# Kernel optimization log

Measured on AMD Instinct MI355X. Metric: run time of the kernel, lower is better.

Reference implementation:

```python
import jax, jax.numpy as jnp
import numpy as np

N_NODES = 200000
N_EDGES = 1000000
N_Q = 64
N_REL_ROWS = 401  # 2*n_rel + 1
D = 128
A = 64


def setup_inputs() -> dict:
    key = jax.random.key(0)
    ks = jax.random.split(key, 16)
    s = 0.05  # param scale
    return {
        'hidden': jax.random.normal(ks[0], (N_NODES, D), jnp.float32),
        'q_emb': jax.random.normal(ks[1], (N_Q, D), jnp.float32),
        'rela_embed': jax.random.normal(ks[2], (N_REL_ROWS, D), jnp.float32),
        'Ws_w': jax.random.normal(ks[3], (A, D), jnp.float32) * s,
        'Ws_b': jax.random.normal(ks[4], (A,), jnp.float32) * s,
        'Wr_w': jax.random.normal(ks[5], (A, D), jnp.float32) * s,
        'Wq_w': jax.random.normal(ks[6], (A, D), jnp.float32) * s,
        'Wqr_w': jax.random.normal(ks[7], (A, D), jnp.float32) * s,
        'walpha_w': jax.random.normal(ks[8], (1, A), jnp.float32) * s,
        'walpha_b': jax.random.normal(ks[9], (1,), jnp.float32) * s,
        'Wh_w': jax.random.normal(ks[10], (D, D), jnp.float32) * s,
        'r_idx': jax.random.randint(ks[11], (N_EDGES,), 0, N_Q, jnp.int32),
        'rel': jax.random.randint(ks[12], (N_EDGES,), 0, N_REL_ROWS, jnp.int32),
        'sub': jax.random.randint(ks[13], (N_EDGES,), 0, N_NODES, jnp.int32),
        'obj': jax.random.randint(ks[14], (N_EDGES,), 0, N_NODES, jnp.int32),
    }


def reference(hidden, q_emb, rela_embed, Ws_w, Ws_b, Wr_w, Wq_w, Wqr_w,
              walpha_w, walpha_b, Wh_w, r_idx, rel, sub, obj):
    # Gather per-edge features (memory-bound irregular access)
    hs = hidden[sub]          # [E, D]
    hr = rela_embed[rel]      # [E, D]
    h_qr = q_emb[r_idx]       # [E, D]

    # Fused small attention MLP: sigmoid(w_alpha(relu(Ws hs + Wr hr + Wq hq + Wqr (hr*hq))))
    pre = (jnp.einsum('ed,ad->ea', hs, Ws_w) + Ws_b
           + jnp.einsum('ed,ad->ea', hr, Wr_w)
           + jnp.einsum('ed,ad->ea', h_qr, Wq_w)
           + jnp.einsum('ed,ad->ea', hr * h_qr, Wqr_w))  # [E, A]
    alpha = jax.nn.sigmoid(jnp.einsum('ea,oa->eo', jax.nn.relu(pre), walpha_w) + walpha_b)  # [E, 1]

    # Gated message + scatter-sum aggregation per target node
    message = alpha * (hs * hr)                                   # [E, D]
    message_agg = jax.ops.segment_sum(message, obj, num_segments=N_NODES)  # [N, D]

    hidden_new = jax.nn.relu(jnp.einsum('nd,od->no', message_agg, Wh_w))   # [N, D]
    return hidden_new, alpha
```

## Files before the change

### kernel.cpp

```cpp
#include <hip/hip_runtime.h>
#include <hip/hip_bf16.h>
#include <hip/hip_fp8.h>

#define N_NODES 200000
#define N_EDGES 1000000
#define NQ 64
#define NRELR 401
#define DIM 128
#define AA 64
#define NBK 3125
#define CAP 512

typedef __attribute__((ext_vector_type(8))) short short8_t;
typedef __attribute__((ext_vector_type(4))) float f32x4;

static __device__ inline short f2bs(float f) {
  __hip_bfloat16 h = __float2bfloat16(f);
  return __builtin_bit_cast(short, h);
}
static __device__ inline float bs2f(unsigned short u) {
  unsigned x = ((unsigned)u) << 16;
  return __builtin_bit_cast(float, x);
}
static __device__ inline unsigned pk2(float lo, float hi) {
  unsigned short a = (unsigned short)__builtin_bit_cast(short, __float2bfloat16(lo));
  unsigned short b = (unsigned short)__builtin_bit_cast(short, __float2bfloat16(hi));
  return (unsigned)a | ((unsigned)b << 16);
}
static __device__ inline unsigned char f2e4(float f) {
  __hip_fp8_e4m3 h(f);
  return (unsigned char)h.__x;
}
static __device__ inline float e42f(unsigned char b) {
  __hip_fp8_e4m3 h;
  h.__x = (__hip_fp8_storage_t)b;
  return (float)h;
}
static __device__ inline void atomic_pk_bf16_s(unsigned voff, unsigned val,
                                               const unsigned short* base) {
  asm volatile("global_atomic_pk_add_bf16 %0, %1, %2"
               :: "v"(voff), "v"(val), "s"((unsigned long long)base) : "memory");
}
static __device__ inline short8_t pack8(float4 a, float4 b) {
  short8_t v;
  v[0] = f2bs(a.x); v[1] = f2bs(a.y); v[2] = f2bs(a.z); v[3] = f2bs(a.w);
  v[4] = f2bs(b.x); v[5] = f2bs(b.y); v[6] = f2bs(b.z); v[7] = f2bs(b.w);
  return v;
}

#define CBK 401
#define SBK 512
__global__ __launch_bounds__(256) void prep_kernel(
    const float* __restrict__ hidden, const float* __restrict__ qemb,
    const float* __restrict__ rela, const float* __restrict__ Ws,
    const float* __restrict__ Wsb, const float* __restrict__ Wr,
    const float* __restrict__ Wq, const float* __restrict__ Wqr,
    const int* __restrict__ obj,
    unsigned char* __restrict__ C8, unsigned char* __restrict__ S8,
    unsigned short* __restrict__ relab, short* __restrict__ hidb,
    int* __restrict__ hist2d, int znum) {
  int b = blockIdx.x;
  int t = threadIdx.x;

  if (b < CBK) {
    __shared__ __hip_bfloat16 hqs[64][136];
    __shared__ __hip_bfloat16 vts[128][72];
    __shared__ float hr_f[128];
    __shared__ float trp[4][64];
    __shared__ float tr_s[64];
    int rho = b;

    if (t < 128) {
      float hv = rela[rho * DIM + t];
      hr_f[t] = hv;
      relab[rho * DIM + t] = (unsigned short)f2bs(hv);
    }
    __syncthreads();
    for (int i = t; i < 64 * 128; i += 256) {
      int q = i >> 7, d = i & 127;
      hqs[q][d] = __float2bfloat16(qemb[i]);
      int a = i >> 7;
      vts[d][a] = __float2bfloat16(Wq[i] + hr_f[d] * Wqr[i]);
    }
    {
      int a = t & 63, qt = t >> 6;
      const float* wr = Wr + a * DIM + qt * 32;
      float p = 0.f;
#pragma unroll 8
      for (int i = 0; i < 32; ++i) p += wr[i] * hr_f[qt * 32 + i];
      trp[qt][a] = p;
    }
    __syncthreads();
    if (t < 64)
      tr_s[t] = trp[0][t] + trp[1][t] + trp[2][t] + trp[3][t] + Wsb[t];
    __syncthreads();

    int qg = t >> 4, ag = t & 15;
    int q0 = qg * 4, a0 = ag * 4;
    float acc[4][4];
#pragma unroll
    for (int i = 0; i < 4; ++i)
#pragma unroll
      for (int j = 0; j < 4; ++j) acc[i][j] = 0.f;
    for (int d = 0; d < DIM; ++d) {
      float hv[4], wv[4];
#pragma unroll
      for (int i = 0; i < 4; ++i) hv[i] = __bfloat162float(hqs[q0 + i][d]);
#pragma unroll
      for (int j = 0; j < 4; ++j) wv[j] = __bfloat162float(vts[d][a0 + j]);
#pragma unroll
      for (int i = 0; i < 4; ++i)
#pragma unroll
        for (int j = 0; j < 4; ++j) acc[i][j] += hv[i] * wv[j];
    }
#pragma unroll
    for (int i = 0; i < 4; ++i)
#pragma unroll
      for (int j = 0; j < 4; ++j) {
        int q = q0 + i, a = a0 + j;
        C8[((size_t)rho * 64 + q) * 64 + a] = f2e4(acc[i][j] + tr_s[a]);
      }
  } else if (b < CBK + SBK) {
    int lane = t & 63;
    int lr = lane & 15, lg = lane >> 4;
    int gw = (b - CBK) * 4 + (t >> 6);
    const int NWV = SBK * 4;

    short8_t bf[4][4];
#pragma unroll
    for (int ot = 0; ot < 4; ++ot)
#pragma unroll
      for (int kt = 0; kt < 4; ++kt) {
        const float* wp = Ws + (size_t)(ot * 16 + lr) * DIM + kt * 32 + lg * 8;
        bf[ot][kt] = pack8(*(const float4*)wp, *(const float4*)(wp + 4));
      }

    for (int tt = gw; tt < N_NODES / 16; tt += NWV) {
      const float* ap = hidden + (size_t)tt * 16 * DIM + (size_t)lr * DIM;
      short8_t a[4];
#pragma unroll
      for (int kt = 0; kt < 4; ++kt) {
        const float* p = ap + kt * 32 + lg * 8;
        a[kt] = pack8(*(const float4*)p, *(const float4*)(p + 4));
        *(short8_t*)(hidb + ((size_t)tt * 16 + lr) * DIM + kt * 32 + lg * 8) = a[kt];
      }
      f32x4 acc[4];
#pragma unroll
      for (int ot = 0; ot < 4; ++ot) {
        acc[ot] = (f32x4){0.f, 0.f, 0.f, 0.f};
#pragma unroll
        for (int kt = 0; kt < 4; ++kt)
          acc[ot] = __builtin_amdgcn_mfma_f32_16x16x32_bf16(a[kt], bf[ot][kt], acc[ot], 0, 0, 0);
      }
#pragma unroll
      for (int ot = 0; ot < 4; ++ot)
#pragma unroll
        for (int r = 0; r < 4; ++r)
          S8[((size_t)tt * 16 + lg * 4 + r) * 64 + ot * 16 + lr] = f2e4(acc[ot][r]);
    }
  } else {
    __shared__ int h[NBK];
    int z = b - CBK - SBK;
    for (int i = t; i < NBK; i += 256) h[i] = 0;
    __syncthreads();
    for (int e = z * 256 + t; e < N_EDGES; e += znum * 256)
      atomicAdd(&h[obj[e] >> 6], 1);
    __syncthreads();
    for (int i = t; i < NBK; i += 256)
      hist2d[(size_t)z * NBK + i] = h[i];
  }
}

__global__ __launch_bounds__(256) void offsetsA_kernel(
    const int* __restrict__ hist2d, int* __restrict__ off2d,
    int* __restrict__ totals, int znum) {
  int b0 = blockIdx.x * 256 + threadIdx.x;
  if (b0 >= NBK) return;
  int run = 0;
  for (int z = 0; z < znum; ++z) {
    int v = hist2d[(size_t)z * NBK + b0];
    off2d[(size_t)z * NBK + b0] = run;
    run += v;
  }
  totals[b0] = run;
}

__global__ __launch_bounds__(256) void scan_kernel(
    const int* __restrict__ totals, int* __restrict__ base) {
  __shared__ int part[256];
  int t = threadIdx.x;
  const int PER = (NBK + 255) / 256;
  int lo = t * PER;
  int loc[PER];
  int s = 0;
#pragma unroll
  for (int k = 0; k < PER; ++k) {
    loc[k] = s;
    int idx = lo + k;
    s += (idx < NBK) ? totals[idx] : 0;
  }
  part[t] = s;
  __syncthreads();
  for (int off = 1; off < 256; off <<= 1) {
    int v = (t >= off) ? part[t - off] : 0;
    __syncthreads();
    part[t] += v;
    __syncthreads();
  }
  int pre = (t == 0) ? 0 : part[t - 1];
#pragma unroll
  for (int k = 0; k < PER; ++k) {
    int idx = lo + k;
    if (idx < NBK) base[idx] = pre + loc[k];
  }
  if (t == 255) base[NBK] = part[255];
}

__global__ __launch_bounds__(256) void scatter3_kernel(
    const int* __restrict__ ridx, const int* __restrict__ rel,
    const int* __restrict__ sub, const int* __restrict__ obj,
    const int* __restrict__ base, const int* __restrict__ off2d,
    uint2* __restrict__ recs, int znum) {
  __shared__ int loff[NBK];
  __shared__ int lcur[NBK];
  int t = threadIdx.x, z = blockIdx.x;
  for (int i = t; i < NBK; i += 256) {
    loff[i] = base[i] + off2d[(size_t)z * NBK + i];
    lcur[i] = 0;
  }
  __syncthreads();
  for (int e = z * 256 + t; e < N_EDGES; e += znum * 256) {
    int s = sub[e], r = rel[e], q = ridx[e], o = obj[e];
    int bb = o >> 6;
    int rq = r * 64 + q;
    int p = loff[bb] + atomicAdd(&lcur[bb], 1);
    uint2 rc;
    rc.x = (unsigned)s | ((unsigned)(o & 63) << 18) | ((unsigned)(rq & 0xFF) << 24);
    rc.y = (unsigned)(rq >> 8) | ((unsigned)e << 7);
    recs[p] = rc;
  }
}

__global__ __launch_bounds__(256) void bucket2_kernel(
    const unsigned* __restrict__ hid32, const unsigned* __restrict__ rel32,
    const unsigned char* __restrict__ S8, const unsigned char* __restrict__ C8,
    const float* __restrict__ wal, const float* __restrict__ walb,
    const int* __restrict__ base, const uint2* __restrict__ recs,
    unsigned* __restrict__ agg32, float* __restrict__ alpha_out) {
  __shared__ uint2 lrec[CAP];
  __shared__ unsigned short ord[CAP];
  __shared__ int cnt2[64];
  __shared__ int scn[65];
  __shared__ int curs[64];
  int t = threadIdx.x, b = blockIdx.x;
  int lane = t & 63, w = t >> 6;
  int lo = base[b], hi = base[b + 1];
  int cnt = hi - lo;
  int nbase = b * 64;
  float wa = wal[lane];
  float wb = walb[0];

  if (t < 64) cnt2[t] = 0;
  __syncthreads();

  if (cnt <= CAP) {
    for (int i = t; i < cnt; i += 256) {
      uint2 rc = recs[lo + i];
      lrec[i] = rc;
      atomicAdd(&cnt2[(rc.x >> 18) & 63], 1);
    }
    __syncthreads();
    if (t < 64) scn[t + 1] = cnt2[t];
    if (t == 0) scn[0] = 0;
    __syncthreads();
    for (int off = 1; off < 64; off <<= 1) {
      int v = 0;
      if (t < 64) { v = scn[t + 1]; if (t + 1 > off) v += scn[t + 1 - off]; }
      __syncthreads();
      if (t < 64) scn[t + 1] = v;
      __syncthreads();
    }
    if (t < 64) curs[t] = scn[t];
    __syncthreads();
    for (int i = t; i < cnt; i += 256) {
      int oin = (lrec[i].x >> 18) & 63;
      int p = atomicAdd(&curs[oin], 1);
      ord[p] = (unsigned short)i;
    }
    __syncthreads();

    int n0 = w * 16;
    int s0 = scn[n0], s1 = scn[n0 + 16];
    float m0 = 0.f, m1 = 0.f;
    int curn = -1;
    for (int j = s0; j < s1; j += 4) {
      int nv = s1 - j;
      if (nv > 4) nv = 4;
      int sdx[4], on[4], rq[4], ei[4];
      float y[4], h0[4], h1[4], g0[4], g1[4];
#pragma unroll
      for (int u = 0; u < 4; ++u) {
        int idx = (u < nv) ? (j + u) : j;
        uint2 rc = lrec[ord[idx]];
        unsigned rx = __builtin_amdgcn_readfirstlane(rc.x);
        unsigned ry = __builtin_amdgcn_readfirstlane(rc.y);
        sdx[u] = rx & 0x3FFFF;
        on[u] = (rx >> 18) & 63;
        rq[u] = ((rx >> 24) & 0xFF) | ((ry & 0x7F) << 8);
        ei[u] = ry >> 7;
      }
#pragma unroll
      for (int u = 0; u < 4; ++u) {
        float x = e42f(S8[(size_t)sdx[u] * 64 + lane]) +
                  e42f(C8[(size_t)rq[u] * 64 + lane]);
        y[u] = fmaxf(x, 0.f) * wa;
      }
#pragma unroll
      for (int u = 0; u < 4; ++u) {
        unsigned hp = hid32[(size_t)sdx[u] * 64 + lane];
        unsigned rp = rel32[(size_t)(rq[u] >> 6) * 64 + lane];
        h0[u] = bs2f((unsigned short)(hp & 0xffff));
        h1[u] = bs2f((unsigned short)(hp >> 16));
        g0[u] = bs2f((unsigned short)(rp & 0xffff));
        g1[u] = bs2f((unsigned short)(rp >> 16));
      }
#pragma unroll
      for (int off = 32; off; off >>= 1) {
#pragma unroll
        for (int u = 0; u < 4; ++u) y[u] += __shfl_xor(y[u], off);
      }
#pragma unroll
      for (int u = 0; u < 4; ++u) {
        if (u < nv) {
          float al = 1.f / (1.f + __expf(-(y[u] + wb)));
          if (on[u] != curn) {
            if (curn >= 0)
              agg32[(size_t)(nbase + curn) * 64 + lane] = pk2(m0, m1);
            curn = on[u];
            m0 = 0.f; m1 = 0.f;
          }
          m0 += al * h0[u] * g0[u];
          m1 += al * h1[u] * g1[u];
          if (lane == 0) alpha_out[ei[u]] = al;
        }
      }
    }
    if (curn >= 0)
      agg32[(size_t)(nbase + curn) * 64 + lane] = pk2(m0, m1);
    for (int n = n0; n < n0 + 16; ++n) {
      if (cnt2[n] == 0)
        agg32[(size_t)(nbase + n) * 64 + lane] = 0u;
    }
  } else {
    for (int n = w; n < 64; n += 4)
      agg32[(size_t)(nbase + n) * 64 + lane] = 0u;
    __syncthreads();
    unsigned voff = (unsigned)lane * 4;
    for (int i = lo + w * 4; i < hi; i += 16) {
      int nv = hi - i;
      if (nv > 4) nv = 4;
      for (int u = 0; u < 4; ++u) {
        if (u >= nv) break;
        uint2 rc = recs[i + u];
        unsigned rx = __builtin_amdgcn_readfirstlane(rc.x);
        unsigned ry = __builtin_amdgcn_readfirstlane(rc.y);
        int sdx = rx & 0x3FFFF;
        int on = (rx >> 18) & 63;
        int rq = ((rx >> 24) & 0xFF) | ((ry & 0x7F) << 8);
        int ei = ry >> 7;
        float x = e42f(S8[(size_t)sdx * 64 + lane]) + e42f(C8[(size_t)rq * 64 + lane]);
        float y = fmaxf(x, 0.f) * wa;
        for (int off = 32; off; off >>= 1) y += __shfl_xor(y, off);
        float al = 1.f / (1.f + __expf(-(y + wb)));
        unsigned hp = hid32[(size_t)sdx * 64 + lane];
        unsigned rp = rel32[(size_t)(rq >> 6) * 64 + lane];
        float v0 = al * bs2f((unsigned short)(hp & 0xffff)) * bs2f((unsigned short)(rp & 0xffff));
        float v1 = al * bs2f((unsigned short)(hp >> 16)) * bs2f((unsigned short)(rp >> 16));
        atomic_pk_bf16_s(voff, pk2(v0, v1), (const unsigned short*)(agg32 + (size_t)(nbase + on) * 64));
        if (lane == 0) alpha_out[ei] = al;
      }
    }
  }
}

__global__ __launch_bounds__(256) void out_gemm_bf(
    const float* __restrict__ Wh, const short* __restrict__ aggb,
    float* __restrict__ out) {
  int lane = threadIdx.x & 63;
  int lr = lane & 15, lg = lane >> 4;
  int gw = (blockIdx.x * blockDim.x + threadIdx.x) >> 6;
  int nwv = (gridDim.x * blockDim.x) >> 6;

  short8_t b[8][4];
#pragma unroll
  for (int ot = 0; ot < 8; ++ot)
#pragma unroll
    for (int kt = 0; kt < 4; ++kt) {
      const float* wp = Wh + (size_t)(ot * 16 + lr) * DIM + kt * 32 + lg * 8;
      b[ot][kt] = pack8(*(const float4*)wp, *(const float4*)(wp + 4));
    }

  for (int t = gw; t < N_NODES / 16; t += nwv) {
    const short* ap = aggb + ((size_t)t * 16 + lr) * DIM;
    short8_t a[4];
#pragma unroll
    for (int kt = 0; kt < 4; ++kt)
      a[kt] = *(const short8_t*)(ap + kt * 32 + lg * 8);
    f32x4 acc[8];
#pragma unroll
    for (int ot = 0; ot < 8; ++ot) {
      acc[ot] = (f32x4){0.f, 0.f, 0.f, 0.f};
#pragma unroll
      for (int kt = 0; kt < 4; ++kt)
        acc[ot] = __builtin_amdgcn_mfma_f32_16x16x32_bf16(a[kt], b[ot][kt], acc[ot], 0, 0, 0);
    }
    float* op = out + (size_t)t * 16 * DIM;
#pragma unroll
    for (int ot = 0; ot < 8; ++ot)
#pragma unroll
      for (int r = 0; r < 4; ++r)
        op[(size_t)(lg * 4 + r) * DIM + ot * 16 + lr] = fmaxf(acc[ot][r], 0.f);
  }
}

__global__ __launch_bounds__(256) void tq_kernel(
    const float* __restrict__ qemb, const float* __restrict__ Wq,
    float* __restrict__ Tq) {
  int t = blockIdx.x * 256 + threadIdx.x;
  if (t >= NQ * AA) return;
  int q = t >> 6, a = t & 63;
  float s = 0.f;
#pragma unroll 4
  for (int d = 0; d < DIM; ++d) s += qemb[q * DIM + d] * Wq[a * DIM + d];
  Tq[t] = s;
}

__global__ __launch_bounds__(256) void build_C_old(
    const float* __restrict__ qemb, const float* __restrict__ rela,
    const float* __restrict__ Wr, const float* __restrict__ Wqr,
    const float* __restrict__ Wsb, const float* __restrict__ Tq,
    __hip_bfloat16* __restrict__ Cout) {
  __shared__ float hrq[64 * 129];
  __shared__ float wqrT[128 * 65];
  __shared__ float wrT[128 * 65];
  __shared__ float hr_s[128];
  __shared__ float tr_s[64];
  int rho = blockIdx.x;
  int t = threadIdx.x;
  if (t < 128) hr_s[t] = rela[rho * DIM + t];
  __syncthreads();
  for (int i = t; i < 64 * 128; i += 256) {
    int a = i >> 7, d = i & 127;
    hrq[a * 129 + d] = qemb[i] * hr_s[d];
    wqrT[d * 65 + a] = Wqr[i];
    wrT[d * 65 + a] = Wr[i];
  }
  __syncthreads();
  if (t < 64) {
    float s = 0.f;
#pragma unroll 4
    for (int d = 0; d < DIM; ++d) s += wrT[d * 65 + t] * hr_s[d];
    tr_s[t] = s + Wsb[t];
  }
  __syncthreads();
  int qg = t >> 4, ag = t & 15;
  int q0 = qg * 4, a0 = ag * 4;
  float acc[4][4];
#pragma unroll
  for (int i = 0; i < 4; ++i)
#pragma unroll
    for (int j = 0; j < 4; ++j) acc[i][j] = 0.f;
  for (int d = 0; d < DIM; ++d) {
    float hv[4], wv[4];
#pragma unroll
    for (int i = 0; i < 4; ++i) hv[i] = hrq[(q0 + i) * 129 + d];
#pragma unroll
    for (int j = 0; j < 4; ++j) wv[j] = wqrT[d * 65 + a0 + j];
#pragma unroll
    for (int i = 0; i < 4; ++i)
#pragma unroll
      for (int j = 0; j < 4; ++j) acc[i][j] += hv[i] * wv[j];
  }
#pragma unroll
  for (int i = 0; i < 4; ++i)
#pragma unroll
    for (int j = 0; j < 4; ++j) {
      int q = q0 + i, a = a0 + j;
      Cout[(rho * 64 + q) * 64 + a] = __float2bfloat16(acc[i][j] + Tq[q * 64 + a] + tr_s[a]);
    }
}

__global__ __launch_bounds__(256) void build_S_old(
    const float* __restrict__ hidden, const float* __restrict__ Ws,
    __hip_bfloat16* __restrict__ Sout) {
  int lane = threadIdx.x & 63;
  int lr = lane & 15, lg = lane >> 4;
  int gw = (blockIdx.x * blockDim.x + threadIdx.x) >> 6;
  int nwv = (gridDim.x * blockDim.x) >> 6;
  short8_t b[4][4];
#pragma unroll
  for (int ot = 0; ot < 4; ++ot)
#pragma unroll
    for (int kt = 0; kt < 4; ++kt) {
      const float* wp = Ws + (size_t)(ot * 16 + lr) * DIM + kt * 32 + lg * 8;
      b[ot][kt] = pack8(*(const float4*)wp, *(const float4*)(wp + 4));
    }
  for (int t = gw; t < N_NODES / 16; t += nwv) {
    const float* ap = hidden + (size_t)t * 16 * DIM + (size_t)lr * DIM;
    short8_t a[4];
#pragma unroll
    for (int kt = 0; kt < 4; ++kt) {
      const float* p = ap + kt * 32 + lg * 8;
      a[kt] = pack8(*(const float4*)p, *(const float4*)(p + 4));
    }
    f32x4 acc[4];
#pragma unroll
    for (int ot = 0; ot < 4; ++ot) {
      acc[ot] = (f32x4){0.f, 0.f, 0.f, 0.f};
#pragma unroll
      for (int kt = 0; kt < 4; ++kt)
        acc[ot] = __builtin_amdgcn_mfma_f32_16x16x32_bf16(a[kt], b[ot][kt], acc[ot], 0, 0, 0);
    }
#pragma unroll
    for (int ot = 0; ot < 4; ++ot)
#pragma unroll
      for (int r = 0; r < 4; ++r)
        Sout[((size_t)t * 16 + lg * 4 + r) * 64 + ot * 16 + lr] = __float2bfloat16(acc[ot][r]);
  }
}

__global__ __launch_bounds__(256) void edge_kernel_old(
    const float* __restrict__ hidden, const float* __restrict__ rela,
    const __hip_bfloat16* __restrict__ S, const __hip_bfloat16* __restrict__ C,
    const float* __restrict__ wal, const float* __restrict__ walb,
    const int* __restrict__ ridx, const int* __restrict__ rel,
    const int* __restrict__ sub, const int* __restrict__ obj,
    float* __restrict__ agg, float* __restrict__ alpha_out) {
  int lane = threadIdx.x & 63;
  int wid = (blockIdx.x * blockDim.x + threadIdx.x) >> 6;
  const int CH = 124;
  int e0 = wid * CH;
  if (e0 >= N_EDGES) return;
  int e1 = e0 + CH;
  if (e1 > N_EDGES) e1 = N_EDGES;
  float wa = wal[lane];
  float wb = walb[0];
  for (int e = e0; e < e1; e += 4) {
    int4 ss = *(const int4*)(sub + e);
    int4 rr = *(const int4*)(rel + e);
    int4 qq = *(const int4*)(ridx + e);
    int4 oo = *(const int4*)(obj + e);
    int s[4] = {ss.x, ss.y, ss.z, ss.w};
    int r[4] = {rr.x, rr.y, rr.z, rr.w};
    int q[4] = {qq.x, qq.y, qq.z, qq.w};
    int o[4] = {oo.x, oo.y, oo.z, oo.w};
    float y[4];
#pragma unroll
    for (int u = 0; u < 4; ++u) {
      float x = __bfloat162float(S[(size_t)s[u] * 64 + lane]) +
                __bfloat162float(C[((size_t)r[u] * 64 + q[u]) * 64 + lane]);
      y[u] = fmaxf(x, 0.f) * wa;
    }
    float h0[4], h1[4], r0[4], r1[4];
#pragma unroll
    for (int u = 0; u < 4; ++u) {
      h0[u] = hidden[(size_t)s[u] * DIM + lane];
      h1[u] = hidden[(size_t)s[u] * DIM + 64 + lane];
      r0[u] = rela[(size_t)r[u] * DIM + lane];
      r1[u] = rela[(size_t)r[u] * DIM + 64 + lane];
    }
#pragma unroll
    for (int off = 32; off; off >>= 1) {
#pragma unroll
      for (int u = 0; u < 4; ++u) y[u] += __shfl_xor(y[u], off);
    }
    float al[4];
#pragma unroll
    for (int u = 0; u < 4; ++u) al[u] = 1.f / (1.f + __expf(-(y[u] + wb)));
#pragma unroll
    for (int u = 0; u < 4; ++u) {
      unsafeAtomicAdd(&agg[(size_t)o[u] * DIM + lane], al[u] * h0[u] * r0[u]);
      unsafeAtomicAdd(&agg[(size_t)o[u] * DIM + 64 + lane], al[u] * h1[u] * r1[u]);
    }
    if (lane == 0)
      *(float4*)(alpha_out + e) = make_float4(al[0], al[1], al[2], al[3]);
  }
}

__global__ __launch_bounds__(256) void out_gemm_old(
    const float* __restrict__ Wh, float* __restrict__ agg) {
  int lane = threadIdx.x & 63;
  int lr = lane & 15, lg = lane >> 4;
  int gw = (blockIdx.x * blockDim.x + threadIdx.x) >> 6;
  int nwv = (gridDim.x * blockDim.x) >> 6;
  short8_t b[8][4];
#pragma unroll
  for (int ot = 0; ot < 8; ++ot)
#pragma unroll
    for (int kt = 0; kt < 4; ++kt) {
      const float* wp = Wh + (size_t)(ot * 16 + lr) * DIM + kt * 32 + lg * 8;
      b[ot][kt] = pack8(*(const float4*)wp, *(const float4*)(wp + 4));
    }
  for (int t = gw; t < N_NODES / 16; t += nwv) {
    float* ap = agg + (size_t)t * 16 * DIM + (size_t)lr * DIM;
    short8_t a[4];
#pragma unroll
    for (int kt = 0; kt < 4; ++kt) {
      const float* p = ap + kt * 32 + lg * 8;
      a[kt] = pack8(*(const float4*)p, *(const float4*)(p + 4));
    }
    f32x4 acc[8];
#pragma unroll
    for (int ot = 0; ot < 8; ++ot) {
      acc[ot] = (f32x4){0.f, 0.f, 0.f, 0.f};
#pragma unroll
      for (int kt = 0; kt < 4; ++kt)
        acc[ot] = __builtin_amdgcn_mfma_f32_16x16x32_bf16(a[kt], b[ot][kt], acc[ot], 0, 0, 0);
    }
    float* op = agg + (size_t)t * 16 * DIM;
#pragma unroll
    for (int ot = 0; ot < 8; ++ot)
#pragma unroll
      for (int r = 0; r < 4; ++r)
        op[(size_t)(lg * 4 + r) * DIM + ot * 16 + lr] = fmaxf(acc[ot][r], 0.f);
  }
}

extern "C" void kernel_launch(void* const* d_in, const int* in_sizes, int n_in,
                              void* d_out, int out_size, void* d_ws, size_t ws_size,
                              hipStream_t stream) {
  const float* hidden = (const float*)d_in[0];
  const float* qemb   = (const float*)d_in[1];
  const float* rela   = (const float*)d_in[2];
  const float* Ws_w   = (const float*)d_in[3];
  const float* Ws_b   = (const float*)d_in[4];
  const float* Wr_w   = (const float*)d_in[5];
  const float* Wq_w   = (const float*)d_in[6];
  const float* Wqr_w  = (const float*)d_in[7];
  const float* wal_w  = (const float*)d_in[8];
  const float* wal_b  = (const float*)d_in[9];
  const float* Wh_w   = (const float*)d_in[10];
  const int* r_idx    = (const int*)d_in[11];
  const int* rel      = (const int*)d_in[12];
  const int* sub      = (const int*)d_in[13];
  const int* obj      = (const int*)d_in[14];

  float* out_hidden = (float*)d_out;
  float* out_alpha  = out_hidden + (size_t)N_NODES * DIM;

  char* ws = (char*)d_ws;
  const size_t OFF_C8  = 0;
  const size_t SZ_C8   = (size_t)NRELR * 64 * 64;
  const size_t OFF_S8  = OFF_C8 + SZ_C8;
  const size_t SZ_S8   = (size_t)N_NODES * 64;
  const size_t OFF_RB  = OFF_S8 + SZ_S8;
  const size_t SZ_RB   = (size_t)NRELR * DIM * 2;
  const size_t OFF_HB  = OFF_RB + SZ_RB;
  const size_t SZ_HB   = (size_t)N_NODES * DIM * 2;
  const size_t OFF_AG  = OFF_HB + SZ_HB;
  const size_t OFF_H2D = OFF_AG + SZ_HB;

  int znum = 0;
  size_t off_o2d = 0, off_tot = 0, off_base = 0, off_rec = 0;
  for (int zc = 256; zc >= 128; zc >>= 1) {
    size_t szh = (size_t)zc * NBK * 4;
    size_t o2d = OFF_H2D + szh;
    size_t tot = o2d + szh;
    size_t bas = tot + 16384;
    size_t rec = bas + 16384;
    size_t need = rec + (size_t)N_EDGES * 8;
    if (ws_size >= need) {
      znum = zc; off_o2d = o2d; off_tot = tot; off_base = bas; off_rec = rec;
      break;
    }
  }

  if (znum) {
    unsigned char* C8 = (unsigned char*)(ws + OFF_C8);
    unsigned char* S8 = (unsigned char*)(ws + OFF_S8);
    unsigned short* relab = (unsigned short*)(ws + OFF_RB);
    short* hidb = (short*)(ws + OFF_HB);
    unsigned short* aggb = (unsigned short*)(ws + OFF_AG);
    int* hist2d = (int*)(ws + OFF_H2D);
    int* off2d  = (int*)(ws + off_o2d);
    int* totals = (int*)(ws + off_tot);
    int* base   = (int*)(ws + off_base);
    uint2* recs = (uint2*)(ws + off_rec);

    prep_kernel<<<CBK + SBK + znum, 256, 0, stream>>>(
        hidden, qemb, rela, Ws_w, Ws_b, Wr_w, Wq_w, Wqr_w, obj,
        C8, S8, relab, hidb, hist2d, znum);
    offsetsA_kernel<<<(NBK + 255) / 256, 256, 0, stream>>>(hist2d, off2d, totals, znum);
    scan_kernel<<<1, 256, 0, stream>>>(totals, base);
    scatter3_kernel<<<znum, 256, 0, stream>>>(r_idx, rel, sub, obj, base, off2d, recs, znum);
    bucket2_kernel<<<NBK, 256, 0, stream>>>(
        (const unsigned*)hidb, (const unsigned*)relab, S8, C8,
        wal_w, wal_b, base, recs, (unsigned*)aggb, out_alpha);
    out_gemm_bf<<<512, 256, 0, stream>>>(Wh_w, (const short*)aggb, out_hidden);
  } else {
    const size_t OFF_CBo = 16384;
    const size_t SZ_CBo  = (size_t)NRELR * 64 * 64 * 2;
    const size_t OFF_SBo = OFF_CBo + SZ_CBo;
    float* Tq = (float*)ws;
    __hip_bfloat16* Cb = (__hip_bfloat16*)(ws + OFF_CBo);
    __hip_bfloat16* Sb = (__hip_bfloat16*)(ws + OFF_SBo);
    hipMemsetAsync(out_hidden, 0, (size_t)N_NODES * DIM * sizeof(float), stream);
    tq_kernel<<<16, 256, 0, stream>>>(qemb, Wq_w, Tq);
    build_C_old<<<NRELR, 256, 0, stream>>>(qemb, rela, Wr_w, Wqr_w, Ws_b, Tq, Cb);
    build_S_old<<<512, 256, 0, stream>>>(hidden, Ws_w, Sb);
    edge_kernel_old<<<2048, 256, 0, stream>>>(hidden, rela, Sb, Cb, wal_w, wal_b,
                                              r_idx, rel, sub, obj, out_hidden, out_alpha);
    out_gemm_old<<<512, 256, 0, stream>>>(Wh_w, out_hidden);
  }
}
```

Measured before the change: 305.6 us.

## Parallelize per-bucket offset scan across a wavefront with shuffle prefix sum

Replaces the offsets kernel, in which one thread serially walked all znum histogram rows per bucket, with one 64-lane wavefront per bucket. Each lane sums up to 4 consecutive rows and a shuffle-based inclusive scan produces the exclusive offsets. The launch grows from 13 blocks to about 782, exposing far more parallelism for this latency-bound step. It assumes znum is a multiple of 64 and at most 256; other values would silently drop rows.

```diff
diff --git a/kernel.cpp b/kernel.cpp
--- a/kernel.cpp
+++ b/kernel.cpp
@@ -171,18 +171,37 @@
   }
 }
 
-__global__ __launch_bounds__(256) void offsetsA_kernel(
+__global__ __launch_bounds__(256) void offsetsB_kernel(
     const int* __restrict__ hist2d, int* __restrict__ off2d,
     int* __restrict__ totals, int znum) {
-  int b0 = blockIdx.x * 256 + threadIdx.x;
-  if (b0 >= NBK) return;
-  int run = 0;
-  for (int z = 0; z < znum; ++z) {
-    int v = hist2d[(size_t)z * NBK + b0];
-    off2d[(size_t)z * NBK + b0] = run;
-    run += v;
-  }
-  totals[b0] = run;
+  int t = threadIdx.x;
+  int lane = t & 63, w = t >> 6;
+  int b = blockIdx.x * 4 + w;
+  if (b >= NBK) return;
+  int n = znum >> 6;
+  int v[4], loc[4];
+  int s = 0;
+#pragma unroll 4
+  for (int j = 0; j < 4; ++j) {
+    if (j < n) {
+      v[j] = hist2d[(size_t)(lane * n + j) * NBK + b];
+      loc[j] = s;
+      s += v[j];
+    }
+  }
+  int x = s;
+#pragma unroll
+  for (int off = 1; off < 64; off <<= 1) {
+    int y = __shfl_up(x, off);
+    if (lane >= off) x += y;
+  }
+  int excl = x - s;
+#pragma unroll 4
+  for (int j = 0; j < 4; ++j) {
+    if (j < n)
+      off2d[(size_t)(lane * n + j) * NBK + b] = excl + loc[j];
+  }
+  if (lane == 63) totals[b] = x;
 }
 
 __global__ __launch_bounds__(256) void scan_kernel(
@@ -690,7 +709,7 @@
     prep_kernel<<<CBK + SBK + znum, 256, 0, stream>>>(
         hidden, qemb, rela, Ws_w, Ws_b, Wr_w, Wq_w, Wqr_w, obj,
         C8, S8, relab, hidb, hist2d, znum);
-    offsetsA_kernel<<<(NBK + 255) / 256, 256, 0, stream>>>(hist2d, off2d, totals, znum);
+    offsetsB_kernel<<<(NBK + 3) / 4, 256, 0, stream>>>(hist2d, off2d, totals, znum);
     scan_kernel<<<1, 256, 0, stream>>>(totals, base);
     scatter3_kernel<<<znum, 256, 0, stream>>>(r_idx, rel, sub, obj, base, off2d, recs, znum);
     bucket2_kernel<<<NBK, 256, 0, stream>>>(
```

After: 255.3 us. 16.5% less time.
